# Kernel tuning notes

Hardware: AMD Instinct MI355X
Metric: run time of the kernel (lower is better)

## Reference

```python
import jax, jax.numpy as jnp
import numpy as np

N_EMBD = 2048
N_HEAD = 16
N_KV_HEAD = 4
HEAD_DIM = N_EMBD // N_HEAD  # 128
BLOCK_SIZE = 2048
B, T = 4, 2048


def _rope_cache(max_pos, head_dim):
    inv_freq = 1.0 / (10000.0 ** (np.arange(0, head_dim, 2, dtype=np.float32) / head_dim))
    t = np.arange(max_pos, dtype=np.float32)
    freqs = np.repeat(np.outer(t, inv_freq), 2, axis=-1)  # [max_pos, head_dim], interleaved repeat
    return jnp.asarray(np.cos(freqs)), jnp.asarray(np.sin(freqs))

COS, SIN = _rope_cache(BLOCK_SIZE, HEAD_DIM)


def _apply_rope(x, pos):
    # x: [B, nh, T, hd]; matches torch module: cos/sin repeat-interleaved, rotate by halves
    Tq = x.shape[2]
    cos = jax.lax.dynamic_slice_in_dim(COS, pos, Tq, axis=0)[None, None]  # [1,1,T,hd]
    sin = jax.lax.dynamic_slice_in_dim(SIN, pos, Tq, axis=0)[None, None]
    hd = x.shape[-1]
    x1, x2 = x[..., : hd // 2], x[..., hd // 2 :]
    return x * cos + jnp.concatenate([-x2, x1], axis=-1) * sin


def setup_inputs() -> dict:
    key = jax.random.key(0)
    ks = jax.random.split(key, 5)
    scale = 1.0 / np.sqrt(N_EMBD)
    return {
        "x": jax.random.normal(ks[0], (B, T, N_EMBD), dtype=jnp.float32),
        "Wq": jax.random.normal(ks[1], (N_EMBD, N_EMBD), dtype=jnp.float32) * scale,
        "Wk": jax.random.normal(ks[2], (N_EMBD, N_KV_HEAD * HEAD_DIM), dtype=jnp.float32) * scale,
        "Wv": jax.random.normal(ks[3], (N_EMBD, N_KV_HEAD * HEAD_DIM), dtype=jnp.float32) * scale,
        "Wo": jax.random.normal(ks[4], (N_EMBD, N_EMBD), dtype=jnp.float32) * scale,
        "pos": 0,
    }


def reference(x, Wq, Wk, Wv, Wo, pos):
    Bx, Tx, C = x.shape
    q = (x @ Wq).reshape(Bx, Tx, N_HEAD, HEAD_DIM).transpose(0, 2, 1, 3)      # [B,nh,T,hd]
    k = (x @ Wk).reshape(Bx, Tx, N_KV_HEAD, HEAD_DIM).transpose(0, 2, 1, 3)   # [B,nkv,T,hd]
    v = (x @ Wv).reshape(Bx, Tx, N_KV_HEAD, HEAD_DIM).transpose(0, 2, 1, 3)
    q = _apply_rope(q, pos)
    k = _apply_rope(k, pos)
    # GQA: expand kv heads to query heads (cache=None -> causal prefill)
    rep = N_HEAD // N_KV_HEAD
    kr = jnp.repeat(k, rep, axis=1)
    vr = jnp.repeat(v, rep, axis=1)
    scores = jnp.einsum("bhqd,bhkd->bhqk", q, kr) / np.sqrt(HEAD_DIM)
    causal = jnp.tril(jnp.ones((Tx, Tx), dtype=bool))
    scores = jnp.where(causal[None, None], scores, jnp.finfo(scores.dtype).min)
    att = jax.nn.softmax(scores, axis=-1)
    out = jnp.einsum("bhqk,bhkd->bhqd", att, vr)          # [B,nh,T,hd]
    y = out.transpose(0, 2, 1, 3).reshape(Bx, Tx, C)
    return y @ Wo
```

## Files before the change

kernel.cpp:

```cpp
#include <hip/hip_runtime.h>
#include <math.h>

#define TT 2048

typedef __attribute__((ext_vector_type(8))) short bfrag;
typedef __attribute__((ext_vector_type(4))) float facc;

#define NEG_BIG (-1.0e30f)

typedef __attribute__((address_space(1))) const void gas_void;
typedef __attribute__((address_space(3))) void las_void;

__device__ __forceinline__ void gl_lds16(const void* g, void* l) {
    __builtin_amdgcn_global_load_lds((gas_void*)g, (las_void*)l, 16, 0, 0);
}

__device__ __forceinline__ unsigned short f2b(float f) {
    union { float f; unsigned int i; } v; v.f = f;
    unsigned int b = v.i;
    return (unsigned short)((b + 0x7FFFu + ((b >> 16) & 1u)) >> 16);
}
__device__ __forceinline__ float b2f(unsigned short s) {
    union { unsigned int i; float f; } u; u.i = ((unsigned int)s) << 16; return u.f;
}
__device__ __forceinline__ void cvt8_f32(const float* __restrict__ p, unsigned short* d) {
    float4 lo = *(const float4*)p, hi = *(const float4*)(p + 4);
    d[0] = f2b(lo.x); d[1] = f2b(lo.y); d[2] = f2b(lo.z); d[3] = f2b(lo.w);
    d[4] = f2b(hi.x); d[5] = f2b(hi.y); d[6] = f2b(hi.z); d[7] = f2b(hi.w);
}

__global__ __launch_bounds__(256) void k_cvt_trig(const float* __restrict__ in,
                                                  unsigned short* __restrict__ out,
                                                  float2* __restrict__ tab,
                                                  const int* __restrict__ posPtr) {
    int bi = blockIdx.x;
    if (bi < 8192) {
        int c = bi * 256 + threadIdx.x;
        unsigned short t[8];
        cvt8_f32(in + (size_t)c * 8, t);
        *(uint4*)(out + (size_t)c * 8) = *(const uint4*)t;
    } else {
        int tid = (bi - 8192) * 256 + threadIdx.x;
        int i1 = tid & 63, t = tid >> 6;
        float p = (float)(*posPtr + t);
        float f = exp2f(-(float)i1 * 0.20762050595278f);
        float th = p * f;
        tab[tid] = make_float2(cosf(th), sinf(th));
    }
}

__global__ __launch_bounds__(256) void k_wt_all(const float* __restrict__ Wq,
                                                const float* __restrict__ Wk,
                                                const float* __restrict__ Wv,
                                                const float* __restrict__ Wo,
                                                unsigned short* __restrict__ WqT,
                                                unsigned short* __restrict__ WkvT,
                                                unsigned short* __restrict__ WoT) {
    __shared__ alignas(16) unsigned short tile[64][72];
    int i = blockIdx.x;
    const float* W; unsigned short* WT; int N, bx, by;
    if (i < 1024)      { W = Wq; WT = WqT; N = 2048; bx = i & 31; by = i >> 5; }
    else if (i < 1280) { int j = i - 1024; W = Wk; WT = WkvT; N = 512; bx = j & 7; by = j >> 3; }
    else if (i < 1536) { int j = i - 1280; W = Wv; WT = WkvT + (size_t)512 * 2048; N = 512; bx = j & 7; by = j >> 3; }
    else               { int j = i - 1536; W = Wo; WT = WoT; N = 2048; bx = j & 31; by = j >> 5; }
    int r0 = by * 64, c0 = bx * 64;
    int tid = threadIdx.x;
    for (int k = 0; k < 2; ++k) {
        int c = tid + k * 256;
        int row = c >> 3, c8 = (c & 7) * 8;
        unsigned short t[8];
        cvt8_f32(W + (size_t)(r0 + row) * N + c0 + c8, t);
        *(uint4*)&tile[row][c8] = *(const uint4*)t;
    }
    __syncthreads();
    for (int k = 0; k < 2; ++k) {
        int c = tid + k * 256;
        int col = c >> 3, r8 = (c & 7) * 8;
        unsigned short t[8];
        for (int j = 0; j < 8; ++j) t[j] = tile[r8 + j][col];
        *(uint4*)(WT + (size_t)(c0 + col) * 2048 + r0 + r8) = *(const uint4*)t;
    }
}

__global__ __launch_bounds__(256) void k_postq(unsigned short* __restrict__ QKV,
                                               unsigned short* __restrict__ VbT,
                                               const float2* __restrict__ tab) {
    __shared__ alignas(16) unsigned short tile[64][72];
    int bi = blockIdx.x;
    if (bi < 20480) {
        unsigned short* X; int lognh, tid;
        if (bi < 16384) { X = QKV;        lognh = 4; tid = bi * 256 + threadIdx.x; }
        else            { X = QKV + 2048; lognh = 2; tid = (bi - 16384) * 256 + threadIdx.x; }
        int d2 = tid & 31;
        int nh = 1 << lognh;
        int h = (tid >> 5) & (nh - 1);
        int row = tid >> (5 + lognh);
        int t = row & (TT - 1);
        size_t base = (size_t)row * 3072 + h * 128 + d2 * 2;
        unsigned int ua = *(const unsigned int*)(X + base);
        unsigned int ub = *(const unsigned int*)(X + base + 64);
        float x1a = b2f((unsigned short)(ua & 0xffff));
        float x1b = b2f((unsigned short)(ua >> 16));
        float x2a = b2f((unsigned short)(ub & 0xffff));
        float x2b = b2f((unsigned short)(ub >> 16));
        float2 cs1 = tab[t * 64 + d2];
        float2 cs2 = tab[t * 64 + d2 + 32];
        unsigned int o1 = (unsigned int)f2b(x1a * cs1.x - x2a * cs1.y)
                        | ((unsigned int)f2b(x1b * cs1.x - x2b * cs1.y) << 16);
        unsigned int o2 = (unsigned int)f2b(x2a * cs2.x + x1a * cs2.y)
                        | ((unsigned int)f2b(x2b * cs2.x + x1b * cs2.y) << 16);
        *(unsigned int*)(X + base)      = o1;
        *(unsigned int*)(X + base + 64) = o2;
    } else {
        int j = bi - 20480;
        int r0 = (j >> 3) * 64, c0 = (j & 7) * 64;
        int tid = threadIdx.x;
        for (int k = 0; k < 2; ++k) {
            int c = tid + k * 256;
            int row = c >> 3, c8 = (c & 7) * 8;
            *(uint4*)&tile[row][c8] =
                *(const uint4*)(QKV + (size_t)(r0 + row) * 3072 + 2560 + c0 + c8);
        }
        __syncthreads();
        for (int k = 0; k < 2; ++k) {
            int c = tid + k * 256;
            int col = c >> 3, r8 = (c & 7) * 8;
            unsigned short t[8];
            for (int jj = 0; jj < 8; ++jj) t[jj] = tile[r8 + jj][col];
            *(uint4*)(VbT + (size_t)(c0 + col) * 8192 + r0 + r8) = *(const uint4*)t;
        }
    }
}

__global__ __launch_bounds__(256) void k_gemm2ph(const unsigned short* __restrict__ A,
                                                 const unsigned short* __restrict__ Bt,
                                                 void* __restrict__ Cmat,
                                                 int M, int N, int K, int outF) {
    __shared__ union SM {
        struct { unsigned short A[2][128][64]; unsigned short B[2][128][64]; } s;
        unsigned short ct[32][136];
        float          ctf[32][136];
    } sm;
    int tid = threadIdx.x;
    int w = tid >> 6, lane = tid & 63, quad = lane >> 4, l15 = lane & 15;
    int m0 = blockIdx.y * 128, n0 = blockIdx.x * 128;
    int wm = (w >> 1) * 64, wn = (w & 1) * 64;

    int srow   = lane >> 3;
    int schunk = (lane & 7) ^ (lane >> 3);

    facc acc[4][4];
#pragma unroll
    for (int mi = 0; mi < 4; ++mi)
#pragma unroll
        for (int ni = 0; ni < 4; ++ni)
#pragma unroll
            for (int r = 0; r < 4; ++r) acc[mi][ni][r] = 0.f;

    auto stage = [&](int bb, int k0) {
#pragma unroll
        for (int i = 0; i < 4; ++i) {
            int row = w * 32 + i * 8;
            gl_lds16(A  + (size_t)(m0 + row + srow) * K + k0 + schunk * 8, &sm.s.A[bb][row][0]);
            gl_lds16(Bt + (size_t)(n0 + row + srow) * K + k0 + schunk * 8, &sm.s.B[bb][row][0]);
        }
    };

    int NT = K >> 6;
    stage(0, 0);
    __syncthreads();

    for (int t = 0; t < NT; ++t) {
        int cur = t & 1;
        if (t + 1 < NT) stage(cur ^ 1, (t + 1) * 64);

        bfrag af[4][2], bf[4][2];
#pragma unroll
        for (int mi = 0; mi < 4; ++mi)
#pragma unroll
            for (int kc = 0; kc < 2; ++kc)
                af[mi][kc] = *(const bfrag*)&sm.s.A[cur][wm + mi * 16 + l15][((kc * 4 + quad) ^ (l15 & 7)) * 8];
#pragma unroll
        for (int ni = 0; ni < 4; ++ni)
#pragma unroll
            for (int kc = 0; kc < 2; ++kc)
                bf[ni][kc] = *(const bfrag*)&sm.s.B[cur][wn + ni * 16 + l15][((kc * 4 + quad) ^ (l15 & 7)) * 8];
#pragma unroll
        for (int kc = 0; kc < 2; ++kc)
#pragma unroll
            for (int mi = 0; mi < 4; ++mi)
#pragma unroll
                for (int ni = 0; ni < 4; ++ni)
                    acc[mi][ni] = __builtin_amdgcn_mfma_f32_16x16x32_bf16(af[mi][kc], bf[ni][kc], acc[mi][ni], 0, 0, 0);

        __syncthreads();
    }

#pragma unroll
    for (int t = 0; t < 4; ++t) {
        __syncthreads();
#pragma unroll
        for (int ni = 0; ni < 4; ++ni)
#pragma unroll
            for (int r = 0; r < 4; ++r) {
                int lr = (w >> 1) * 16 + quad * 4 + r;
                int lc = wn + ni * 16 + l15;
                if (outF) sm.ctf[lr][lc] = acc[t][ni][r];
                else      sm.ct [lr][lc] = f2b(acc[t][ni][r]);
            }
        __syncthreads();
        if (outF) {
#pragma unroll
            for (int i = 0; i < 4; ++i) {
                int cc = tid + i * 256;
                int lr = cc >> 5, c4 = (cc & 31) * 4;
                int grow = m0 + (lr >> 4) * 64 + t * 16 + (lr & 15);
                *(float4*)((float*)Cmat + (size_t)grow * N + n0 + c4) =
                    *(const float4*)&sm.ctf[lr][c4];
            }
        } else {
#pragma unroll
            for (int i = 0; i < 2; ++i) {
                int cc = tid + i * 256;
                int lr = cc >> 4, c8 = (cc & 15) * 8;
                int grow = m0 + (lr >> 4) * 64 + t * 16 + (lr & 15);
                *(uint4*)((unsigned short*)Cmat + (size_t)grow * N + n0 + c8) =
                    *(const uint4*)&sm.ct[lr][c8];
            }
        }
    }
}

__device__ __forceinline__ void flash_pass(
    int qbase, int b, int h, int kvh,
    const unsigned short* __restrict__ QKV,
    const unsigned short* __restrict__ VbT,
    unsigned short* __restrict__ att,
    unsigned short (&Ks)[2][32][136],
    unsigned short (&Vt)[2][128][40],
    unsigned short (&Pt)[8][16][40]) {

    int tid = threadIdx.x;
    int w = tid >> 6, lane = tid & 63, quad = lane >> 4, l15 = lane & 15;

    bfrag qf[4];
    {
        size_t qrow = (size_t)(b * TT + qbase + w * 16 + l15);
        for (int kc = 0; kc < 4; ++kc)
            qf[kc] = *(const bfrag*)(QKV + qrow * 3072 + h * 128 + kc * 32 + quad * 8);
    }

    float mreg = NEG_BIG, lreg = 0.f;
    facc o[8];
#pragma unroll
    for (int nb2 = 0; nb2 < 8; ++nb2)
#pragma unroll
        for (int r = 0; r < 4; ++r) o[nb2][r] = 0.f;

    int krow = tid >> 4, d8 = (tid & 15) * 8;
    int vd = tid >> 2, tc = (tid & 3) * 8;
    const unsigned short* Kg = QKV + (size_t)(b * TT) * 3072 + 2048 + kvh * 128;
    const unsigned short* Vg = VbT + (size_t)(kvh * 128 + vd) * 8192 + b * TT;

    const float sc = 0.08838834764831845f;
    int kmax = qbase + 128;
    int nt = kmax >> 5;
    int qgmin = qbase + w * 16;
    int myq = qgmin + l15;

    uint4 rk = *(const uint4*)(Kg + (size_t)krow * 3072 + d8);
    uint4 rv = *(const uint4*)(Vg + tc);

    for (int t = 0; t < nt; ++t) {
        int cur = t & 1;
        int k0 = t * 32;
        *(uint4*)&Ks[cur][krow][d8] = rk;
        *(uint4*)&Vt[cur][vd][tc]   = rv;
        __syncthreads();

        if (t + 1 < nt) {
            int k0n = k0 + 32;
            rk = *(const uint4*)(Kg + (size_t)(k0n + krow) * 3072 + d8);
            rv = *(const uint4*)(Vg + k0n + tc);
        }

        if (k0 > qgmin + 15) continue;

        facc s[2];
#pragma unroll
        for (int nb = 0; nb < 2; ++nb) {
#pragma unroll
            for (int r = 0; r < 4; ++r) s[nb][r] = 0.f;
#pragma unroll
            for (int kc = 0; kc < 4; ++kc) {
                bfrag kf = *(const bfrag*)&Ks[cur][nb * 16 + l15][kc * 32 + quad * 8];
                s[nb] = __builtin_amdgcn_mfma_f32_16x16x32_bf16(kf, qf[kc], s[nb], 0, 0, 0);
            }
        }

        bool fullT = (k0 + 31) <= qgmin;
        float v[2][4];
        if (fullT) {
#pragma unroll
            for (int nb = 0; nb < 2; ++nb)
#pragma unroll
                for (int r = 0; r < 4; ++r) v[nb][r] = s[nb][r] * sc;
        } else {
#pragma unroll
            for (int nb = 0; nb < 2; ++nb)
#pragma unroll
                for (int r = 0; r < 4; ++r) {
                    int kg = k0 + nb * 16 + quad * 4 + r;
                    v[nb][r] = (kg > myq) ? NEG_BIG : s[nb][r] * sc;
                }
        }

        float mx = fmaxf(fmaxf(fmaxf(v[0][0], v[0][1]), fmaxf(v[0][2], v[0][3])),
                         fmaxf(fmaxf(v[1][0], v[1][1]), fmaxf(v[1][2], v[1][3])));
        mx = fmaxf(mx, __shfl_xor(mx, 16, 64));
        mx = fmaxf(mx, __shfl_xor(mx, 32, 64));

        bool need = (mx > mreg + 8.f);
        float mnew = need ? mx : mreg;
        float alpha = need ? __expf(mreg - mnew) : 1.f;

        float p[2][4];
        float psum = 0.f;
#pragma unroll
        for (int nb = 0; nb < 2; ++nb)
#pragma unroll
            for (int r = 0; r < 4; ++r) {
                p[nb][r] = __expf(v[nb][r] - mnew);
                psum += p[nb][r];
            }
        psum += __shfl_xor(psum, 16, 64);
        psum += __shfl_xor(psum, 32, 64);
        lreg = lreg * alpha + psum;
        mreg = mnew;

#pragma unroll
        for (int nb = 0; nb < 2; ++nb) {
            unsigned short pk[4];
#pragma unroll
            for (int r = 0; r < 4; ++r) pk[r] = f2b(p[nb][r]);
            *(uint2*)&Pt[w][l15][nb * 16 + quad * 4] = *(const uint2*)pk;
        }

        if (__any(need)) {
#pragma unroll
            for (int r = 0; r < 4; ++r) {
                float al = __shfl(alpha, quad * 4 + r, 16);
#pragma unroll
                for (int nb2 = 0; nb2 < 8; ++nb2) o[nb2][r] *= al;
            }
        }

        asm volatile("s_waitcnt lgkmcnt(0)" ::: "memory");
        bfrag pf = *(const bfrag*)&Pt[w][l15][quad * 8];
#pragma unroll
        for (int nb2 = 0; nb2 < 8; ++nb2) {
            bfrag vf = *(const bfrag*)&Vt[cur][nb2 * 16 + l15][quad * 8];
            o[nb2] = __builtin_amdgcn_mfma_f32_16x16x32_bf16(pf, vf, o[nb2], 0, 0, 0);
        }
    }

    float lr[4];
#pragma unroll
    for (int r = 0; r < 4; ++r) lr[r] = __shfl(lreg, quad * 4 + r, 16);
#pragma unroll
    for (int nb2 = 0; nb2 < 8; ++nb2)
#pragma unroll
        for (int r = 0; r < 4; ++r) {
            int qg = qbase + w * 16 + quad * 4 + r;
            att[(size_t)(b * TT + qg) * 2048 + h * 128 + nb2 * 16 + l15] =
                f2b(o[nb2][r] / lr[r]);
        }
}

__global__ __launch_bounds__(512, 4) void k_flash(const unsigned short* __restrict__ QKV,
                                                  const unsigned short* __restrict__ VbT,
                                                  unsigned short* __restrict__ att) {
    __shared__ alignas(16) unsigned short Ks[2][32][136];
    __shared__ alignas(16) unsigned short Vt[2][128][40];
    __shared__ alignas(16) unsigned short Pt[8][16][40];
    int bh = blockIdx.y;
    int b = bh >> 4, h = bh & 15;
    int kvh = h >> 2;
    int i = blockIdx.x;

    flash_pass(i * 128, b, h, kvh, QKV, VbT, att, Ks, Vt, Pt);
    __syncthreads();
    flash_pass((15 - i) * 128, b, h, kvh, QKV, VbT, att, Ks, Vt, Pt);
}

extern "C" void kernel_launch(void* const* d_in, const int* in_sizes, int n_in,
                              void* d_out, int out_size, void* d_ws, size_t ws_size,
                              hipStream_t stream) {
    const float* x  = (const float*)d_in[0];
    const float* Wq = (const float*)d_in[1];
    const float* Wk = (const float*)d_in[2];
    const float* Wv = (const float*)d_in[3];
    const float* Wo = (const float*)d_in[4];
    const int* pos  = (const int*)d_in[5];

    char* ws = (char*)d_ws;
    unsigned short* xb   = (unsigned short*)(ws + 0);
    unsigned short* QKV  = (unsigned short*)(ws + 33554432);
    unsigned short* VbT  = (unsigned short*)(ws + 83886080);
    unsigned short* WqT  = (unsigned short*)(ws + 92274688);
    unsigned short* WkvT = (unsigned short*)(ws + 100663296);
    unsigned short* WoT  = (unsigned short*)(ws + 104857600);
    float2*         tab  = (float2*)(ws + 113246208);

    k_cvt_trig<<<8704, 256, 0, stream>>>(x, xb, tab, pos);

    k_wt_all<<<2560, 256, 0, stream>>>(Wq, Wk, Wv, Wo, WqT, WkvT, WoT);

    k_gemm2ph<<<dim3(24, 64), 256, 0, stream>>>(xb, WqT, QKV, 8192, 3072, 2048, 0);

    k_postq<<<21504, 256, 0, stream>>>(QKV, VbT, tab);

    k_flash<<<dim3(8, 64), 512, 0, stream>>>(QKV, VbT, xb);

    k_gemm2ph<<<dim3(16, 64), 256, 0, stream>>>(xb, WoT, d_out, 8192, 2048, 2048, 1);
}
```

Baseline: 565.4 us.

## Fuse RoPE into QKV GEMM epilogue and merge preprocessing kernels

Applies the rotary embedding to the Q and K columns inside the QKV GEMM's bf16 store epilogue, using the partner half-row already held in shared memory. This removes the separate read-modify-write RoPE pass over Q and K. The input conversion, trig-table and weight-transpose kernels are merged into one launch, and the V transpose becomes its own small kernel. The trade-off is extra table loads and ALU work in the GEMM epilogue, plus one extra template instantiation.

```diff
diff --git a/kernel.cpp b/kernel.cpp
--- a/kernel.cpp
+++ b/kernel.cpp
@@ -29,113 +29,86 @@
     d[4] = f2b(hi.x); d[5] = f2b(hi.y); d[6] = f2b(hi.z); d[7] = f2b(hi.w);
 }
 
-__global__ __launch_bounds__(256) void k_cvt_trig(const float* __restrict__ in,
-                                                  unsigned short* __restrict__ out,
-                                                  float2* __restrict__ tab,
-                                                  const int* __restrict__ posPtr) {
+__global__ __launch_bounds__(256) void k_pre(const float* __restrict__ x,
+                                             unsigned short* __restrict__ xb,
+                                             float2* __restrict__ tab,
+                                             const int* __restrict__ posPtr,
+                                             const float* __restrict__ Wq,
+                                             const float* __restrict__ Wk,
+                                             const float* __restrict__ Wv,
+                                             const float* __restrict__ Wo,
+                                             unsigned short* __restrict__ WqT,
+                                             unsigned short* __restrict__ WkvT,
+                                             unsigned short* __restrict__ WoT) {
+    __shared__ alignas(16) unsigned short tile[64][72];
     int bi = blockIdx.x;
     if (bi < 8192) {
         int c = bi * 256 + threadIdx.x;
         unsigned short t[8];
-        cvt8_f32(in + (size_t)c * 8, t);
-        *(uint4*)(out + (size_t)c * 8) = *(const uint4*)t;
-    } else {
+        cvt8_f32(x + (size_t)c * 8, t);
+        *(uint4*)(xb + (size_t)c * 8) = *(const uint4*)t;
+    } else if (bi < 8704) {
         int tid = (bi - 8192) * 256 + threadIdx.x;
         int i1 = tid & 63, t = tid >> 6;
         float p = (float)(*posPtr + t);
         float f = exp2f(-(float)i1 * 0.20762050595278f);
         float th = p * f;
         tab[tid] = make_float2(cosf(th), sinf(th));
-    }
-}
-
-__global__ __launch_bounds__(256) void k_wt_all(const float* __restrict__ Wq,
-                                                const float* __restrict__ Wk,
-                                                const float* __restrict__ Wv,
-                                                const float* __restrict__ Wo,
-                                                unsigned short* __restrict__ WqT,
-                                                unsigned short* __restrict__ WkvT,
-                                                unsigned short* __restrict__ WoT) {
+    } else {
+        int i = bi - 8704;
+        const float* W; unsigned short* WT; int N, bx, by;
+        if (i < 1024)      { W = Wq; WT = WqT; N = 2048; bx = i & 31; by = i >> 5; }
+        else if (i < 1280) { int j = i - 1024; W = Wk; WT = WkvT; N = 512; bx = j & 7; by = j >> 3; }
+        else if (i < 1536) { int j = i - 1280; W = Wv; WT = WkvT + (size_t)512 * 2048; N = 512; bx = j & 7; by = j >> 3; }
+        else               { int j = i - 1536; W = Wo; WT = WoT; N = 2048; bx = j & 31; by = j >> 5; }
+        int r0 = by * 64, c0 = bx * 64;
+        int tid = threadIdx.x;
+        for (int k = 0; k < 2; ++k) {
+            int c = tid + k * 256;
+            int row = c >> 3, c8 = (c & 7) * 8;
+            unsigned short t[8];
+            cvt8_f32(W + (size_t)(r0 + row) * N + c0 + c8, t);
+            *(uint4*)&tile[row][c8] = *(const uint4*)t;
+        }
+        __syncthreads();
+        for (int k = 0; k < 2; ++k) {
+            int c = tid + k * 256;
+            int col = c >> 3, r8 = (c & 7) * 8;
+            unsigned short t[8];
+            for (int j = 0; j < 8; ++j) t[j] = tile[r8 + j][col];
+            *(uint4*)(WT + (size_t)(c0 + col) * 2048 + r0 + r8) = *(const uint4*)t;
+        }
+    }
+}
+
+__global__ __launch_bounds__(256) void k_vt(const unsigned short* __restrict__ QKV,
+                                            unsigned short* __restrict__ VbT) {
     __shared__ alignas(16) unsigned short tile[64][72];
-    int i = blockIdx.x;
-    const float* W; unsigned short* WT; int N, bx, by;
-    if (i < 1024)      { W = Wq; WT = WqT; N = 2048; bx = i & 31; by = i >> 5; }
-    else if (i < 1280) { int j = i - 1024; W = Wk; WT = WkvT; N = 512; bx = j & 7; by = j >> 3; }
-    else if (i < 1536) { int j = i - 1280; W = Wv; WT = WkvT + (size_t)512 * 2048; N = 512; bx = j & 7; by = j >> 3; }
-    else               { int j = i - 1536; W = Wo; WT = WoT; N = 2048; bx = j & 31; by = j >> 5; }
-    int r0 = by * 64, c0 = bx * 64;
+    int j = blockIdx.x;
+    int r0 = (j >> 3) * 64, c0 = (j & 7) * 64;
     int tid = threadIdx.x;
     for (int k = 0; k < 2; ++k) {
         int c = tid + k * 256;
         int row = c >> 3, c8 = (c & 7) * 8;
-        unsigned short t[8];
-        cvt8_f32(W + (size_t)(r0 + row) * N + c0 + c8, t);
-        *(uint4*)&tile[row][c8] = *(const uint4*)t;
+        *(uint4*)&tile[row][c8] =
+            *(const uint4*)(QKV + (size_t)(r0 + row) * 3072 + 2560 + c0 + c8);
     }
     __syncthreads();
     for (int k = 0; k < 2; ++k) {
         int c = tid + k * 256;
         int col = c >> 3, r8 = (c & 7) * 8;
         unsigned short t[8];
-        for (int j = 0; j < 8; ++j) t[j] = tile[r8 + j][col];
-        *(uint4*)(WT + (size_t)(c0 + col) * 2048 + r0 + r8) = *(const uint4*)t;
-    }
-}
-
-__global__ __launch_bounds__(256) void k_postq(unsigned short* __restrict__ QKV,
-                                               unsigned short* __restrict__ VbT,
-                                               const float2* __restrict__ tab) {
-    __shared__ alignas(16) unsigned short tile[64][72];
-    int bi = blockIdx.x;
-    if (bi < 20480) {
-        unsigned short* X; int lognh, tid;
-        if (bi < 16384) { X = QKV;        lognh = 4; tid = bi * 256 + threadIdx.x; }
-        else            { X = QKV + 2048; lognh = 2; tid = (bi - 16384) * 256 + threadIdx.x; }
-        int d2 = tid & 31;
-        int nh = 1 << lognh;
-        int h = (tid >> 5) & (nh - 1);
-        int row = tid >> (5 + lognh);
-        int t = row & (TT - 1);
-        size_t base = (size_t)row * 3072 + h * 128 + d2 * 2;
-        unsigned int ua = *(const unsigned int*)(X + base);
-        unsigned int ub = *(const unsigned int*)(X + base + 64);
-        float x1a = b2f((unsigned short)(ua & 0xffff));
-        float x1b = b2f((unsigned short)(ua >> 16));
-        float x2a = b2f((unsigned short)(ub & 0xffff));
-        float x2b = b2f((unsigned short)(ub >> 16));
-        float2 cs1 = tab[t * 64 + d2];
-        float2 cs2 = tab[t * 64 + d2 + 32];
-        unsigned int o1 = (unsigned int)f2b(x1a * cs1.x - x2a * cs1.y)
-                        | ((unsigned int)f2b(x1b * cs1.x - x2b * cs1.y) << 16);
-        unsigned int o2 = (unsigned int)f2b(x2a * cs2.x + x1a * cs2.y)
-                        | ((unsigned int)f2b(x2b * cs2.x + x1b * cs2.y) << 16);
-        *(unsigned int*)(X + base)      = o1;
-        *(unsigned int*)(X + base + 64) = o2;
-    } else {
-        int j = bi - 20480;
-        int r0 = (j >> 3) * 64, c0 = (j & 7) * 64;
-        int tid = threadIdx.x;
-        for (int k = 0; k < 2; ++k) {
-            int c = tid + k * 256;
-            int row = c >> 3, c8 = (c & 7) * 8;
-            *(uint4*)&tile[row][c8] =
-                *(const uint4*)(QKV + (size_t)(r0 + row) * 3072 + 2560 + c0 + c8);
-        }
-        __syncthreads();
-        for (int k = 0; k < 2; ++k) {
-            int c = tid + k * 256;
-            int col = c >> 3, r8 = (c & 7) * 8;
-            unsigned short t[8];
-            for (int jj = 0; jj < 8; ++jj) t[jj] = tile[r8 + jj][col];
-            *(uint4*)(VbT + (size_t)(c0 + col) * 8192 + r0 + r8) = *(const uint4*)t;
-        }
-    }
-}
-
+        for (int jj = 0; jj < 8; ++jj) t[jj] = tile[r8 + jj][col];
+        *(uint4*)(VbT + (size_t)(c0 + col) * 8192 + r0 + r8) = *(const uint4*)t;
+    }
+}
+
+template <int ROPE>
 __global__ __launch_bounds__(256) void k_gemm2ph(const unsigned short* __restrict__ A,
                                                  const unsigned short* __restrict__ Bt,
                                                  void* __restrict__ Cmat,
-                                                 int M, int N, int K, int outF) {
+                                                 int M, int N, int K, int outF,
+                                                 const float2* __restrict__ tab) {
     __shared__ union SM {
         struct { unsigned short A[2][128][64]; unsigned short B[2][128][64]; } s;
         unsigned short ct[32][136];
@@ -224,8 +197,27 @@
                 int cc = tid + i * 256;
                 int lr = cc >> 4, c8 = (cc & 15) * 8;
                 int grow = m0 + (lr >> 4) * 64 + t * 16 + (lr & 15);
-                *(uint4*)((unsigned short*)Cmat + (size_t)grow * N + n0 + c8) =
-                    *(const uint4*)&sm.ct[lr][c8];
+                uint4 val = *(const uint4*)&sm.ct[lr][c8];
+                if constexpr (ROPE) {
+                    if (n0 < 2560) {
+                        unsigned short prt[8];
+                        *(uint4*)prt = *(const uint4*)&sm.ct[lr][c8 ^ 64];
+                        unsigned short* sp = (unsigned short*)&val;
+                        int tt = grow & (TT - 1);
+                        int d = (n0 + c8) & 127;
+                        int hi = d & 64;
+                        const float2* tb = tab + tt * 64 + ((d & 63) >> 1) + (hi ? 32 : 0);
+                        float2 cs0 = tb[0], cs1 = tb[1], cs2 = tb[2], cs3 = tb[3];
+                        float2 cs[4] = {cs0, cs1, cs2, cs3};
+#pragma unroll
+                        for (int j = 0; j < 8; ++j) {
+                            float a = b2f(sp[j]), bq = b2f(prt[j]);
+                            float c = cs[j >> 1].x, s = cs[j >> 1].y;
+                            sp[j] = f2b(hi ? (a * c + bq * s) : (a * c - bq * s));
+                        }
+                    }
+                }
+                *(uint4*)((unsigned short*)Cmat + (size_t)grow * N + n0 + c8) = val;
             }
         }
     }
@@ -412,15 +404,13 @@
     unsigned short* WoT  = (unsigned short*)(ws + 104857600);
     float2*         tab  = (float2*)(ws + 113246208);
 
-    k_cvt_trig<<<8704, 256, 0, stream>>>(x, xb, tab, pos);
-
-    k_wt_all<<<2560, 256, 0, stream>>>(Wq, Wk, Wv, Wo, WqT, WkvT, WoT);
-
-    k_gemm2ph<<<dim3(24, 64), 256, 0, stream>>>(xb, WqT, QKV, 8192, 3072, 2048, 0);
-
-    k_postq<<<21504, 256, 0, stream>>>(QKV, VbT, tab);
+    k_pre<<<11264, 256, 0, stream>>>(x, xb, tab, pos, Wq, Wk, Wv, Wo, WqT, WkvT, WoT);
+
+    k_gemm2ph<1><<<dim3(24, 64), 256, 0, stream>>>(xb, WqT, QKV, 8192, 3072, 2048, 0, tab);
+
+    k_vt<<<1024, 256, 0, stream>>>(QKV, VbT);
 
     k_flash<<<dim3(8, 64), 512, 0, stream>>>(QKV, VbT, xb);
 
-    k_gemm2ph<<<dim3(16, 64), 256, 0, stream>>>(xb, WoT, d_out, 8192, 2048, 2048, 1);
-}
+    k_gemm2ph<0><<<dim3(16, 64), 256, 0, stream>>>(xb, WoT, d_out, 8192, 2048, 2048, 1, nullptr);
+}
```

Result: no change. 557.5 us (-1.4%).
